# Optimization experiments

Hardware: AMD Instinct MI355X
Metric: run time of the kernel (lower is better)

The kernel has to match this reference:

```python
import jax, jax.numpy as jnp
import numpy as np

B, N, C, K = 2, 20000, 256, 16
H = C // 2  # gate hidden

def _ln(x, g, b, eps=1e-5):
    m = jnp.mean(x, axis=-1, keepdims=True)
    v = jnp.mean((x - m) ** 2, axis=-1, keepdims=True)
    return (x - m) * jax.lax.rsqrt(v + eps) * g + b

def setup_inputs() -> dict:
    key = jax.random.key(0)
    ks = jax.random.split(key, 16)
    s = 0.02
    return {
        'x_l0': jax.random.normal(ks[0], (B, N, C), jnp.float32),
        'x_l1': jax.random.normal(ks[1], (B, N, C), jnp.float32),
        'x_l2': jax.random.normal(ks[2], (B, N, C), jnp.float32),
        'x_l3': jax.random.normal(ks[3], (B, N, C), jnp.float32),
        'knn_idx': jax.random.randint(ks[4], (N, K), 0, N, jnp.int32),
        'Wq': jax.random.normal(ks[5], (3, C, C), jnp.float32) * s,
        'bq': jnp.zeros((3, C), jnp.float32),
        'Wk': jax.random.normal(ks[6], (3, C, C), jnp.float32) * s,
        'bk': jnp.zeros((3, C), jnp.float32),
        'Wv': jax.random.normal(ks[7], (3, C, C), jnp.float32) * s,
        'bv': jnp.zeros((3, C), jnp.float32),
        'ln_g': jnp.ones((3, C), jnp.float32),
        'ln_b': jnp.zeros((3, C), jnp.float32),
        'Wg1': jax.random.normal(ks[8], (H, C), jnp.float32) * s,
        'bg1': jnp.zeros((H,), jnp.float32),
        'Wg2': jax.random.normal(ks[9], (3, H), jnp.float32) * s,
        'bg2': jnp.zeros((3,), jnp.float32),
        'fn_g': jnp.ones((C,), jnp.float32),
        'fn_b': jnp.zeros((C,), jnp.float32),
    }

def reference(x_l0, x_l1, x_l2, x_l3, knn_idx, Wq, bq, Wk, bk, Wv, bv,
              ln_g, ln_b, Wg1, bg1, Wg2, bg2, fn_g, fn_b):
    c = x_l3.shape[-1]
    scale = 1.0 / jnp.sqrt(jnp.asarray(c, x_l3.dtype))

    def block(xq, i):
        Q = xq @ Wq[i].T + bq[i]            # (B,N,C)
        Kf = x_l3 @ Wk[i].T + bk[i]         # (B,N,C)
        Vf = x_l3 @ Wv[i].T + bv[i]
        Kk = Kf[:, knn_idx]                 # (B,N,K,C) gather along node dim
        Vk = Vf[:, knn_idx]
        s = jnp.einsum('bnc,bnkc->bnk', Q, Kk) * scale
        a = jax.nn.softmax(s, axis=-1)
        o = jnp.einsum('bnk,bnkc->bnc', a, Vk)
        return _ln(o + Q, ln_g[i], ln_b[i])

    Os = [block(x, i) for i, x in enumerate((x_l0, x_l1, x_l2))]
    h = jax.nn.relu(x_l3 @ Wg1.T + bg1)
    alpha = jax.nn.softmax(h @ Wg2.T + bg2, axis=-1)  # (B,N,3)
    out = sum(alpha[..., i:i + 1] * Os[i] for i in range(3))
    return _ln(out + x_l3, fn_g, fn_b)
```

## Files before the change

### kernel.cpp

```cpp
#include <hip/hip_runtime.h>

#define B_ 2
#define N_ 20000
#define C_ 256
#define K_ 16
#define H_ 128
#define ROWS (B_ * N_)
#define MT 313
#define MPAD (MT * 128)

typedef __attribute__((ext_vector_type(8))) short bf16x8;
typedef __attribute__((ext_vector_type(4))) float f32x4;

__device__ __forceinline__ float us2f(unsigned short u) {
    return __uint_as_float(((unsigned int)u) << 16);
}
__device__ __forceinline__ unsigned short f2us(float f) {
    unsigned int u = __float_as_uint(f);
    unsigned int r = (u + 0x7fffu + ((u >> 16) & 1u)) >> 16;
    return (unsigned short)r;
}
__device__ __forceinline__ float wred(float v) {
#pragma unroll
    for (int off = 32; off > 0; off >>= 1) v += __shfl_xor(v, off, 64);
    return v;
}
__device__ __forceinline__ void gld_lds16(const unsigned short* g, unsigned short* l) {
    __builtin_amdgcn_global_load_lds(
        (__attribute__((address_space(1))) void*)(g),
        (__attribute__((address_space(3))) void*)(l), 16, 0, 0);
}

extern "C" __global__ void __launch_bounds__(256)
cvt_kernel(const float* __restrict__ src, unsigned short* __restrict__ dst, int n4) {
    int t = blockIdx.x * 256 + threadIdx.x;
    if (t >= n4) return;
    float4 v = ((const float4*)src)[t];
    ushort4 o;
    o.x = f2us(v.x); o.y = f2us(v.y); o.z = f2us(v.z); o.w = f2us(v.w);
    ((ushort4*)dst)[t] = o;
}

extern "C" __global__ void __launch_bounds__(256)
cvtw_kernel(const float* __restrict__ s0, const float* __restrict__ s1,
            const float* __restrict__ s2, const float* __restrict__ s3,
            unsigned short* __restrict__ d0, unsigned short* __restrict__ d1,
            unsigned short* __restrict__ d2, unsigned short* __restrict__ d3) {
    const int y = blockIdx.y;
    const float* src = (y == 0) ? s0 : (y == 1 ? s1 : (y == 2 ? s2 : s3));
    unsigned short* dst = (y == 0) ? d0 : (y == 1 ? d1 : (y == 2 ? d2 : d3));
    const int n4 = (y < 3) ? (3 * C_ * C_ / 4) : (H_ * C_ / 4);
    int t = blockIdx.x * 256 + threadIdx.x;
    if (t >= n4) return;
    float4 v = ((const float4*)src)[t];
    ushort4 o;
    o.x = f2us(v.x); o.y = f2us(v.y); o.z = f2us(v.z); o.w = f2us(v.w);
    ((ushort4*)dst)[t] = o;
}

extern "C" __global__ void __launch_bounds__(256)
gemm_bf16(const unsigned short* __restrict__ A0, const unsigned short* __restrict__ A12,
          const unsigned short* __restrict__ W0, const unsigned short* __restrict__ W1,
          const unsigned short* __restrict__ W2, const float* __restrict__ b0,
          const float* __restrict__ b1, const float* __restrict__ b2,
          unsigned short* __restrict__ O0, unsigned short* __restrict__ O1,
          unsigned short* __restrict__ O2, const int Mvalid, const int ldo) {
    const int z = blockIdx.z;
    const unsigned short* A = (z == 0) ? A0 : A12;
    const unsigned short* W = (z == 0) ? W0 : (z == 1 ? W1 : W2);
    const float* bias = (z == 0) ? b0 : (z == 1 ? b1 : b2);
    unsigned short* O = (z == 0) ? O0 : (z == 1 ? O1 : O2);

    const int m0 = blockIdx.x * 128;
    const int n0 = blockIdx.y * 128;
    const int tid = threadIdx.x;
    const int w = tid >> 6, lane = tid & 63;
    const int l15 = lane & 15, l4 = lane >> 4;
    const int rowq = (w >> 1) * 64;
    const int colq = (w & 1) * 64;

    __shared__ unsigned short As[128 * 32];
    __shared__ unsigned short Bs[128 * 32];

    f32x4 acc[4][4] = {};

    const int srow = w * 16 + (lane >> 2);
    const int schunk = (lane & 3) * 8;

    for (int k0 = 0; k0 < 256; k0 += 32) {
        __syncthreads();
#pragma unroll
        for (int issue = 0; issue < 2; ++issue) {
            const int ra = m0 + issue * 64 + srow;
            const int rb = n0 + issue * 64 + srow;
            gld_lds16(A + (size_t)ra * 256 + k0 + schunk, As + issue * 2048 + w * 512);
            gld_lds16(W + (size_t)rb * 256 + k0 + schunk, Bs + issue * 2048 + w * 512);
        }
        __syncthreads();
        bf16x8 a[4], b[4];
#pragma unroll
        for (int i = 0; i < 4; ++i)
            a[i] = *(const bf16x8*)&As[(rowq + i * 16 + l15) * 32 + l4 * 8];
#pragma unroll
        for (int j = 0; j < 4; ++j)
            b[j] = *(const bf16x8*)&Bs[(colq + j * 16 + l15) * 32 + l4 * 8];
#pragma unroll
        for (int i = 0; i < 4; ++i)
#pragma unroll
            for (int j = 0; j < 4; ++j)
                acc[i][j] = __builtin_amdgcn_mfma_f32_16x16x32_bf16(a[i], b[j], acc[i][j], 0, 0, 0);
    }

#pragma unroll
    for (int j = 0; j < 4; ++j) {
        const int gcol = n0 + colq + j * 16 + l15;
        const float bj = bias[gcol];
#pragma unroll
        for (int i = 0; i < 4; ++i) {
#pragma unroll
            for (int r = 0; r < 4; ++r) {
                const int grow = m0 + rowq + i * 16 + l4 * 4 + r;
                if (grow < Mvalid) O[(size_t)grow * ldo + gcol] = f2us(acc[i][j][r] + bj);
            }
        }
    }
}

extern "C" __global__ void __launch_bounds__(256)
gate2_kernel(const unsigned short* __restrict__ Hbf, const float* __restrict__ Wg2,
             const float* __restrict__ bg2, float* __restrict__ alpha) {
    const int tid = threadIdx.x;
    const int w = tid >> 6, lane = tid & 63;
    const int row = blockIdx.x * 4 + w;
    const float h0 = fmaxf(us2f(Hbf[(size_t)row * H_ + lane]), 0.f);
    const float h1 = fmaxf(us2f(Hbf[(size_t)row * H_ + 64 + lane]), 0.f);
    float lg[3];
#pragma unroll
    for (int l = 0; l < 3; ++l) {
        const float* w2 = Wg2 + l * H_;
        lg[l] = wred(h0 * w2[lane] + h1 * w2[lane + 64]) + bg2[l];
    }
    float m = fmaxf(lg[0], fmaxf(lg[1], lg[2]));
    float e0 = expf(lg[0] - m), e1 = expf(lg[1] - m), e2 = expf(lg[2] - m);
    float inv = 1.f / (e0 + e1 + e2);
    if (lane == 0) {
        alpha[row * 3 + 0] = e0 * inv;
        alpha[row * 3 + 1] = e1 * inv;
        alpha[row * 3 + 2] = e2 * inv;
    }
}

extern "C" __global__ void __launch_bounds__(256)
attn_kernel(const unsigned short* __restrict__ q, const unsigned short* __restrict__ kf,
            const unsigned short* __restrict__ vf, const int* __restrict__ knn,
            const float* __restrict__ alpha, const float* __restrict__ lng,
            const float* __restrict__ lnb, float* __restrict__ accum, const int iblk) {
    const int tid = threadIdx.x;
    const int g = tid >> 4;
    const int t = tid & 15;
    const int row = blockIdx.x * 16 + g;
    const int b = row / N_;
    const int n = row - b * N_;

    float qv[16];
    const unsigned short* qp = q + (size_t)row * C_ + t * 4;
#pragma unroll
    for (int j = 0; j < 4; ++j) {
        ushort4 u = *(const ushort4*)(qp + j * 64);
        qv[j * 4 + 0] = us2f(u.x);
        qv[j * 4 + 1] = us2f(u.y);
        qv[j * 4 + 2] = us2f(u.z);
        qv[j * 4 + 3] = us2f(u.w);
    }

    int idxs[K_];
    float s[K_];
#pragma unroll
    for (int k = 0; k < K_; ++k) {
        idxs[k] = knn[n * K_ + k];
        const unsigned short* kp = kf + ((size_t)b * N_ + idxs[k]) * C_ + t * 4;
        float p = 0.f;
#pragma unroll
        for (int j = 0; j < 4; ++j) {
            ushort4 u = *(const ushort4*)(kp + j * 64);
            p += qv[j * 4 + 0] * us2f(u.x) + qv[j * 4 + 1] * us2f(u.y) +
                 qv[j * 4 + 2] * us2f(u.z) + qv[j * 4 + 3] * us2f(u.w);
        }
#pragma unroll
        for (int off = 1; off < 16; off <<= 1) p += __shfl_xor(p, off, 64);
        s[k] = p * 0.0625f;
    }

    float m = s[0];
#pragma unroll
    for (int k = 1; k < K_; ++k) m = fmaxf(m, s[k]);
    float sum = 0.f;
#pragma unroll
    for (int k = 0; k < K_; ++k) {
        s[k] = __expf(s[k] - m);
        sum += s[k];
    }
    const float inv = 1.f / sum;

    float o[16] = {};
#pragma unroll
    for (int k = 0; k < K_; ++k) {
        const float a = s[k] * inv;
        const unsigned short* vp = vf + ((size_t)b * N_ + idxs[k]) * C_ + t * 4;
#pragma unroll
        for (int j = 0; j < 4; ++j) {
            ushort4 u = *(const ushort4*)(vp + j * 64);
            o[j * 4 + 0] += a * us2f(u.x);
            o[j * 4 + 1] += a * us2f(u.y);
            o[j * 4 + 2] += a * us2f(u.z);
            o[j * 4 + 3] += a * us2f(u.w);
        }
    }

    float r[16];
    float s1 = 0.f, s2 = 0.f;
#pragma unroll
    for (int c = 0; c < 16; ++c) {
        r[c] = o[c] + qv[c];
        s1 += r[c];
        s2 += r[c] * r[c];
    }
#pragma unroll
    for (int off = 1; off < 16; off <<= 1) {
        s1 += __shfl_xor(s1, off, 64);
        s2 += __shfl_xor(s2, off, 64);
    }
    const float mean = s1 * (1.f / C_);
    const float var = s2 * (1.f / C_) - mean * mean;
    const float rstd = rsqrtf(var + 1e-5f);

    const float a = alpha[row * 3 + iblk];
    const float* gp = lng + iblk * C_ + t * 4;
    const float* bp = lnb + iblk * C_ + t * 4;
    float* ap = accum + (size_t)row * C_ + t * 4;
#pragma unroll
    for (int j = 0; j < 4; ++j) {
        float4 gg = *(const float4*)(gp + j * 64);
        float4 bb = *(const float4*)(bp + j * 64);
        float4 y;
        y.x = ((r[j * 4 + 0] - mean) * rstd * gg.x + bb.x) * a;
        y.y = ((r[j * 4 + 1] - mean) * rstd * gg.y + bb.y) * a;
        y.z = ((r[j * 4 + 2] - mean) * rstd * gg.z + bb.z) * a;
        y.w = ((r[j * 4 + 3] - mean) * rstd * gg.w + bb.w) * a;
        if (iblk == 0) {
            *(float4*)(ap + j * 64) = y;
        } else {
            float4 p = *(const float4*)(ap + j * 64);
            p.x += y.x; p.y += y.y; p.z += y.z; p.w += y.w;
            *(float4*)(ap + j * 64) = p;
        }
    }
}

extern "C" __global__ void __launch_bounds__(256)
final_kernel(float* __restrict__ accum, const float* __restrict__ x3,
             const float* __restrict__ fng, const float* __restrict__ fnb) {
    const int tid = threadIdx.x;
    const int w = tid >> 6, lane = tid & 63;
    const int row = blockIdx.x * 4 + w;
    const int c0 = lane * 4;
    float4 a = *(const float4*)(accum + (size_t)row * C_ + c0);
    float4 xv = *(const float4*)(x3 + (size_t)row * C_ + c0);
    float4 r = make_float4(a.x + xv.x, a.y + xv.y, a.z + xv.z, a.w + xv.w);
    float s1 = wred(r.x + r.y + r.z + r.w);
    float s2 = wred(r.x * r.x + r.y * r.y + r.z * r.z + r.w * r.w);
    const float mean = s1 * (1.f / C_);
    const float var = s2 * (1.f / C_) - mean * mean;
    const float rstd = rsqrtf(var + 1e-5f);
    const float* g = fng + c0;
    const float* bb = fnb + c0;
    float4 y;
    y.x = (r.x - mean) * rstd * g[0] + bb[0];
    y.y = (r.y - mean) * rstd * g[1] + bb[1];
    y.z = (r.z - mean) * rstd * g[2] + bb[2];
    y.w = (r.w - mean) * rstd * g[3] + bb[3];
    *(float4*)(accum + (size_t)row * C_ + c0) = y;
}

extern "C" void kernel_launch(void* const* d_in, const int* in_sizes, int n_in,
                              void* d_out, int out_size, void* d_ws, size_t ws_size,
                              hipStream_t stream) {
    const float* x0 = (const float*)d_in[0];
    const float* x1 = (const float*)d_in[1];
    const float* x2 = (const float*)d_in[2];
    const float* x3 = (const float*)d_in[3];
    const int* knn = (const int*)d_in[4];
    const float* Wq = (const float*)d_in[5];
    const float* bq = (const float*)d_in[6];
    const float* Wk = (const float*)d_in[7];
    const float* bk = (const float*)d_in[8];
    const float* Wv = (const float*)d_in[9];
    const float* bv = (const float*)d_in[10];
    const float* ln_g = (const float*)d_in[11];
    const float* ln_b = (const float*)d_in[12];
    const float* Wg1 = (const float*)d_in[13];
    const float* bg1 = (const float*)d_in[14];
    const float* Wg2 = (const float*)d_in[15];
    const float* bg2 = (const float*)d_in[16];
    const float* fn_g = (const float*)d_in[17];
    const float* fn_b = (const float*)d_in[18];
    float* out = (float*)d_out;

    unsigned char* w8 = (unsigned char*)d_ws;
    const size_t XBF = (size_t)MPAD * C_ * 2;
    const size_t HBF = (size_t)MPAD * H_ * 2;
    const size_t WBLOB = (size_t)3 * C_ * C_ * 2;
    unsigned short* x3bf = (unsigned short*)(w8);
    unsigned short* xqbf = (unsigned short*)(w8 + XBF);
    unsigned short* qbf  = (unsigned short*)(w8 + 2 * XBF);
    unsigned short* kbf  = (unsigned short*)(w8 + 3 * XBF);
    unsigned short* vbf  = (unsigned short*)(w8 + 4 * XBF);
    unsigned short* Hbf  = (unsigned short*)(w8 + 5 * XBF);
    unsigned short* wqbf = (unsigned short*)(w8 + 5 * XBF + HBF);
    unsigned short* wkbf = (unsigned short*)(w8 + 5 * XBF + HBF + WBLOB);
    unsigned short* wvbf = (unsigned short*)(w8 + 5 * XBF + HBF + 2 * WBLOB);
    unsigned short* wg1bf = (unsigned short*)(w8 + 5 * XBF + HBF + 3 * WBLOB);
    float* alpha = (float*)(w8 + 5 * XBF + HBF + 3 * WBLOB + (size_t)H_ * C_ * 2);

    const int xn4 = ROWS * C_ / 4;
    const int wn4 = 3 * C_ * C_ / 4;

    cvt_kernel<<<(xn4 + 255) / 256, 256, 0, stream>>>(x3, x3bf, xn4);
    cvtw_kernel<<<dim3((wn4 + 255) / 256, 4), 256, 0, stream>>>(
        Wq, Wk, Wv, Wg1, wqbf, wkbf, wvbf, wg1bf);

    gemm_bf16<<<dim3(MT, 1, 1), 256, 0, stream>>>(
        x3bf, x3bf, wg1bf, wg1bf, wg1bf, bg1, bg1, bg1, Hbf, Hbf, Hbf, ROWS, H_);
    gate2_kernel<<<ROWS / 4, 256, 0, stream>>>(Hbf, Wg2, bg2, alpha);

    const float* xq[3] = {x0, x1, x2};
    for (int i = 0; i < 3; ++i) {
        cvt_kernel<<<(xn4 + 255) / 256, 256, 0, stream>>>(xq[i], xqbf, xn4);
        gemm_bf16<<<dim3(MT, 2, 3), 256, 0, stream>>>(
            xqbf, x3bf, wqbf + (size_t)i * C_ * C_, wkbf + (size_t)i * C_ * C_,
            wvbf + (size_t)i * C_ * C_, bq + i * C_, bk + i * C_, bv + i * C_,
            qbf, kbf, vbf, ROWS, C_);
        attn_kernel<<<ROWS / 16, 256, 0, stream>>>(qbf, kbf, vbf, knn, alpha,
                                                   ln_g, ln_b, out, i);
    }
    final_kernel<<<ROWS / 4, 256, 0, stream>>>(out, x3, fn_g, fn_b);
}
```

Measured before the change: 672.8 us.

## Fuse three attention blocks and final layernorm into one gather kernel

Stores Q/K/V for all three blocks in separate workspace slices so a single attn3 kernel can process all three blocks per row. The kernel accumulates the alpha-weighted layernormed outputs in registers and applies the final residual layernorm directly. This removes the fp32 read-modify-write of the output accumulator across three passes and the separate final kernel launch. It also reuses the loaded neighbour indices and uses 8-wide bf16 loads. The cost is roughly twice the workspace, and the old path is kept as a fallback when the workspace is too small.

```diff
diff --git a/kernel.cpp b/kernel.cpp
--- a/kernel.cpp
+++ b/kernel.cpp
@@ -10,6 +10,7 @@
 #define MPAD (MT * 128)
 
 typedef __attribute__((ext_vector_type(8))) short bf16x8;
+typedef __attribute__((ext_vector_type(8))) unsigned short us8;
 typedef __attribute__((ext_vector_type(4))) float f32x4;
 
 __device__ __forceinline__ float us2f(unsigned short u) {
@@ -147,6 +148,174 @@
         alpha[row * 3 + 0] = e0 * inv;
         alpha[row * 3 + 1] = e1 * inv;
         alpha[row * 3 + 2] = e2 * inv;
+    }
+}
+
+extern "C" __global__ void __launch_bounds__(256)
+attn3_kernel(const unsigned short* __restrict__ qb, const unsigned short* __restrict__ kb,
+             const unsigned short* __restrict__ vb, const int* __restrict__ knn,
+             const float* __restrict__ alpha, const float* __restrict__ lng,
+             const float* __restrict__ lnb, const float* __restrict__ x3,
+             const float* __restrict__ fng, const float* __restrict__ fnb,
+             float* __restrict__ out) {
+    const int tid = threadIdx.x;
+    const int t = tid & 15;
+    const int row = blockIdx.x * 16 + (tid >> 4);
+    const int b = row / N_;
+    const int n = row - b * N_;
+    const int XE = MPAD * C_;
+
+    int goff[K_];
+    {
+        const int4* kn = (const int4*)(knn + n * K_);
+#pragma unroll
+        for (int k4 = 0; k4 < 4; ++k4) {
+            int4 v = kn[k4];
+            const int base = b * N_;
+            goff[k4 * 4 + 0] = (base + v.x) * C_ + t * 8;
+            goff[k4 * 4 + 1] = (base + v.y) * C_ + t * 8;
+            goff[k4 * 4 + 2] = (base + v.z) * C_ + t * 8;
+            goff[k4 * 4 + 3] = (base + v.w) * C_ + t * 8;
+        }
+    }
+
+    float acc[16] = {};
+
+#pragma unroll 1
+    for (int i = 0; i < 3; ++i) {
+        const unsigned short* q  = qb + (size_t)i * XE;
+        const unsigned short* kf = kb + (size_t)i * XE;
+        const unsigned short* vf = vb + (size_t)i * XE;
+
+        float qv[16];
+        const unsigned short* qp = q + (size_t)row * C_ + t * 8;
+#pragma unroll
+        for (int j = 0; j < 2; ++j) {
+            us8 u = *(const us8*)(qp + j * 128);
+#pragma unroll
+            for (int e = 0; e < 8; ++e) qv[j * 8 + e] = us2f(u[e]);
+        }
+
+        float s[K_];
+#pragma unroll
+        for (int k = 0; k < K_; ++k) {
+            const unsigned short* kp = kf + goff[k];
+            float p = 0.f;
+#pragma unroll
+            for (int j = 0; j < 2; ++j) {
+                us8 u = *(const us8*)(kp + j * 128);
+#pragma unroll
+                for (int e = 0; e < 8; ++e) p += qv[j * 8 + e] * us2f(u[e]);
+            }
+#pragma unroll
+            for (int off = 1; off < 16; off <<= 1) p += __shfl_xor(p, off, 64);
+            s[k] = p * 0.0625f;
+        }
+
+        float m = s[0];
+#pragma unroll
+        for (int k = 1; k < K_; ++k) m = fmaxf(m, s[k]);
+        float sum = 0.f;
+#pragma unroll
+        for (int k = 0; k < K_; ++k) {
+            s[k] = __expf(s[k] - m);
+            sum += s[k];
+        }
+        const float inv = 1.f / sum;
+
+        float o[16] = {};
+#pragma unroll
+        for (int k = 0; k < K_; ++k) {
+            const float a = s[k] * inv;
+            const unsigned short* vp = vf + goff[k];
+#pragma unroll
+            for (int j = 0; j < 2; ++j) {
+                us8 u = *(const us8*)(vp + j * 128);
+#pragma unroll
+                for (int e = 0; e < 8; ++e) o[j * 8 + e] += a * us2f(u[e]);
+            }
+        }
+
+        float s1 = 0.f, s2 = 0.f;
+#pragma unroll
+        for (int c = 0; c < 16; ++c) {
+            o[c] += qv[c];
+            s1 += o[c];
+            s2 += o[c] * o[c];
+        }
+#pragma unroll
+        for (int off = 1; off < 16; off <<= 1) {
+            s1 += __shfl_xor(s1, off, 64);
+            s2 += __shfl_xor(s2, off, 64);
+        }
+        const float mean = s1 * (1.f / C_);
+        const float var = s2 * (1.f / C_) - mean * mean;
+        const float rstd = rsqrtf(var + 1e-5f);
+
+        const float a = alpha[row * 3 + i];
+        const float* gp = lng + i * C_ + t * 8;
+        const float* bp = lnb + i * C_ + t * 8;
+#pragma unroll
+        for (int j = 0; j < 2; ++j) {
+#pragma unroll
+            for (int h = 0; h < 2; ++h) {
+                float4 gg = *(const float4*)(gp + j * 128 + h * 4);
+                float4 bb = *(const float4*)(bp + j * 128 + h * 4);
+                const int ci = j * 8 + h * 4;
+                acc[ci + 0] += ((o[ci + 0] - mean) * rstd * gg.x + bb.x) * a;
+                acc[ci + 1] += ((o[ci + 1] - mean) * rstd * gg.y + bb.y) * a;
+                acc[ci + 2] += ((o[ci + 2] - mean) * rstd * gg.z + bb.z) * a;
+                acc[ci + 3] += ((o[ci + 3] - mean) * rstd * gg.w + bb.w) * a;
+            }
+        }
+    }
+
+    const float* xp = x3 + (size_t)row * C_ + t * 8;
+    float r[16];
+    float s1 = 0.f, s2 = 0.f;
+#pragma unroll
+    for (int j = 0; j < 2; ++j) {
+#pragma unroll
+        for (int h = 0; h < 2; ++h) {
+            float4 xv = *(const float4*)(xp + j * 128 + h * 4);
+            const int ci = j * 8 + h * 4;
+            r[ci + 0] = acc[ci + 0] + xv.x;
+            r[ci + 1] = acc[ci + 1] + xv.y;
+            r[ci + 2] = acc[ci + 2] + xv.z;
+            r[ci + 3] = acc[ci + 3] + xv.w;
+        }
+    }
+#pragma unroll
+    for (int c = 0; c < 16; ++c) {
+        s1 += r[c];
+        s2 += r[c] * r[c];
+    }
+#pragma unroll
+    for (int off = 1; off < 16; off <<= 1) {
+        s1 += __shfl_xor(s1, off, 64);
+        s2 += __shfl_xor(s2, off, 64);
+    }
+    const float mean = s1 * (1.f / C_);
+    const float var = s2 * (1.f / C_) - mean * mean;
+    const float rstd = rsqrtf(var + 1e-5f);
+
+    const float* gp = fng + t * 8;
+    const float* bp = fnb + t * 8;
+    float* op = out + (size_t)row * C_ + t * 8;
+#pragma unroll
+    for (int j = 0; j < 2; ++j) {
+#pragma unroll
+        for (int h = 0; h < 2; ++h) {
+            float4 gg = *(const float4*)(gp + j * 128 + h * 4);
+            float4 bb = *(const float4*)(bp + j * 128 + h * 4);
+            const int ci = j * 8 + h * 4;
+            float4 y;
+            y.x = (r[ci + 0] - mean) * rstd * gg.x + bb.x;
+            y.y = (r[ci + 1] - mean) * rstd * gg.y + bb.y;
+            y.z = (r[ci + 2] - mean) * rstd * gg.z + bb.z;
+            y.w = (r[ci + 3] - mean) * rstd * gg.w + bb.w;
+            *(float4*)(op + j * 128 + h * 4) = y;
+        }
     }
 }
 
@@ -310,38 +479,76 @@
     const size_t XBF = (size_t)MPAD * C_ * 2;
     const size_t HBF = (size_t)MPAD * H_ * 2;
     const size_t WBLOB = (size_t)3 * C_ * C_ * 2;
-    unsigned short* x3bf = (unsigned short*)(w8);
-    unsigned short* xqbf = (unsigned short*)(w8 + XBF);
-    unsigned short* qbf  = (unsigned short*)(w8 + 2 * XBF);
-    unsigned short* kbf  = (unsigned short*)(w8 + 3 * XBF);
-    unsigned short* vbf  = (unsigned short*)(w8 + 4 * XBF);
-    unsigned short* Hbf  = (unsigned short*)(w8 + 5 * XBF);
-    unsigned short* wqbf = (unsigned short*)(w8 + 5 * XBF + HBF);
-    unsigned short* wkbf = (unsigned short*)(w8 + 5 * XBF + HBF + WBLOB);
-    unsigned short* wvbf = (unsigned short*)(w8 + 5 * XBF + HBF + 2 * WBLOB);
-    unsigned short* wg1bf = (unsigned short*)(w8 + 5 * XBF + HBF + 3 * WBLOB);
-    float* alpha = (float*)(w8 + 5 * XBF + HBF + 3 * WBLOB + (size_t)H_ * C_ * 2);
+    const size_t WG1B = (size_t)H_ * C_ * 2;
+    const size_t ALPHAB = (size_t)ROWS * 3 * 4;
 
     const int xn4 = ROWS * C_ / 4;
     const int wn4 = 3 * C_ * C_ / 4;
-
-    cvt_kernel<<<(xn4 + 255) / 256, 256, 0, stream>>>(x3, x3bf, xn4);
-    cvtw_kernel<<<dim3((wn4 + 255) / 256, 4), 256, 0, stream>>>(
-        Wq, Wk, Wv, Wg1, wqbf, wkbf, wvbf, wg1bf);
-
-    gemm_bf16<<<dim3(MT, 1, 1), 256, 0, stream>>>(
-        x3bf, x3bf, wg1bf, wg1bf, wg1bf, bg1, bg1, bg1, Hbf, Hbf, Hbf, ROWS, H_);
-    gate2_kernel<<<ROWS / 4, 256, 0, stream>>>(Hbf, Wg2, bg2, alpha);
-
     const float* xq[3] = {x0, x1, x2};
-    for (int i = 0; i < 3; ++i) {
-        cvt_kernel<<<(xn4 + 255) / 256, 256, 0, stream>>>(xq[i], xqbf, xn4);
-        gemm_bf16<<<dim3(MT, 2, 3), 256, 0, stream>>>(
-            xqbf, x3bf, wqbf + (size_t)i * C_ * C_, wkbf + (size_t)i * C_ * C_,
-            wvbf + (size_t)i * C_ * C_, bq + i * C_, bk + i * C_, bv + i * C_,
-            qbf, kbf, vbf, ROWS, C_);
-        attn_kernel<<<ROWS / 16, 256, 0, stream>>>(qbf, kbf, vbf, knn, alpha,
-                                                   ln_g, ln_b, out, i);
-    }
-    final_kernel<<<ROWS / 4, 256, 0, stream>>>(out, x3, fn_g, fn_b);
-}
+
+    const size_t NEED_FUSED = 11 * XBF + HBF + 3 * WBLOB + WG1B + ALPHAB;
+
+    if (ws_size >= NEED_FUSED) {
+        unsigned short* x3bf = (unsigned short*)(w8);
+        unsigned short* xqbf = (unsigned short*)(w8 + XBF);
+        unsigned short* qbf  = (unsigned short*)(w8 + 2 * XBF);
+        unsigned short* kbf  = (unsigned short*)(w8 + 5 * XBF);
+        unsigned short* vbf  = (unsigned short*)(w8 + 8 * XBF);
+        unsigned short* Hbf  = (unsigned short*)(w8 + 11 * XBF);
+        unsigned short* wqbf = (unsigned short*)(w8 + 11 * XBF + HBF);
+        unsigned short* wkbf = (unsigned short*)(w8 + 11 * XBF + HBF + WBLOB);
+        unsigned short* wvbf = (unsigned short*)(w8 + 11 * XBF + HBF + 2 * WBLOB);
+        unsigned short* wg1bf = (unsigned short*)(w8 + 11 * XBF + HBF + 3 * WBLOB);
+        float* alpha = (float*)(w8 + 11 * XBF + HBF + 3 * WBLOB + WG1B);
+        const size_t XE = (size_t)MPAD * C_;
+
+        cvt_kernel<<<(xn4 + 255) / 256, 256, 0, stream>>>(x3, x3bf, xn4);
+        cvtw_kernel<<<dim3((wn4 + 255) / 256, 4), 256, 0, stream>>>(
+            Wq, Wk, Wv, Wg1, wqbf, wkbf, wvbf, wg1bf);
+
+        gemm_bf16<<<dim3(MT, 1, 1), 256, 0, stream>>>(
+            x3bf, x3bf, wg1bf, wg1bf, wg1bf, bg1, bg1, bg1, Hbf, Hbf, Hbf, ROWS, H_);
+        gate2_kernel<<<ROWS / 4, 256, 0, stream>>>(Hbf, Wg2, bg2, alpha);
+
+        for (int i = 0; i < 3; ++i) {
+            cvt_kernel<<<(xn4 + 255) / 256, 256, 0, stream>>>(xq[i], xqbf, xn4);
+            gemm_bf16<<<dim3(MT, 2, 3), 256, 0, stream>>>(
+                xqbf, x3bf, wqbf + (size_t)i * C_ * C_, wkbf + (size_t)i * C_ * C_,
+                wvbf + (size_t)i * C_ * C_, bq + i * C_, bk + i * C_, bv + i * C_,
+                qbf + i * XE, kbf + i * XE, vbf + i * XE, ROWS, C_);
+        }
+        attn3_kernel<<<ROWS / 16, 256, 0, stream>>>(qbf, kbf, vbf, knn, alpha,
+                                                    ln_g, ln_b, x3, fn_g, fn_b, out);
+    } else {
+        unsigned short* x3bf = (unsigned short*)(w8);
+        unsigned short* xqbf = (unsigned short*)(w8 + XBF);
+        unsigned short* qbf  = (unsigned short*)(w8 + 2 * XBF);
+        unsigned short* kbf  = (unsigned short*)(w8 + 3 * XBF);
+        unsigned short* vbf  = (unsigned short*)(w8 + 4 * XBF);
+        unsigned short* Hbf  = (unsigned short*)(w8 + 5 * XBF);
+        unsigned short* wqbf = (unsigned short*)(w8 + 5 * XBF + HBF);
+        unsigned short* wkbf = (unsigned short*)(w8 + 5 * XBF + HBF + WBLOB);
+        unsigned short* wvbf = (unsigned short*)(w8 + 5 * XBF + HBF + 2 * WBLOB);
+        unsigned short* wg1bf = (unsigned short*)(w8 + 5 * XBF + HBF + 3 * WBLOB);
+        float* alpha = (float*)(w8 + 5 * XBF + HBF + 3 * WBLOB + WG1B);
+
+        cvt_kernel<<<(xn4 + 255) / 256, 256, 0, stream>>>(x3, x3bf, xn4);
+        cvtw_kernel<<<dim3((wn4 + 255) / 256, 4), 256, 0, stream>>>(
+            Wq, Wk, Wv, Wg1, wqbf, wkbf, wvbf, wg1bf);
+
+        gemm_bf16<<<dim3(MT, 1, 1), 256, 0, stream>>>(
+            x3bf, x3bf, wg1bf, wg1bf, wg1bf, bg1, bg1, bg1, Hbf, Hbf, Hbf, ROWS, H_);
+        gate2_kernel<<<ROWS / 4, 256, 0, stream>>>(Hbf, Wg2, bg2, alpha);
+
+        for (int i = 0; i < 3; ++i) {
+            cvt_kernel<<<(xn4 + 255) / 256, 256, 0, stream>>>(xq[i], xqbf, xn4);
+            gemm_bf16<<<dim3(MT, 2, 3), 256, 0, stream>>>(
+                xqbf, x3bf, wqbf + (size_t)i * C_ * C_, wkbf + (size_t)i * C_ * C_,
+                wvbf + (size_t)i * C_ * C_, bq + i * C_, bk + i * C_, bv + i * C_,
+                qbf, kbf, vbf, ROWS, C_);
+            attn_kernel<<<ROWS / 16, 256, 0, stream>>>(qbf, kbf, vbf, knn, alpha,
+                                                       ln_g, ln_b, out, i);
+        }
+        final_kernel<<<ROWS / 4, 256, 0, stream>>>(out, x3, fn_g, fn_b);
+    }
+}
```

Measured after the change: 910.5 us. 35.3% more time.

## Batch input conversions, fuse final layernorm into last attention pass

Applied to the files above, without the earlier changes.

Converts x3 and all three query inputs to bf16 in one 2D-grid launch instead of four separate launches, using extra workspace for the three query buffers. The final layernorm (residual add with x3 and the fn_g/fn_b normalisation) moves into the third attention kernel, which removes a separate read-modify-write pass over the output. Two attention variants get different minimum-occupancy launch bounds (6 and 5 waves), which may cap registers and cause spills. The workspace footprint grows by two activation-sized buffers.

```diff
diff --git a/kernel.cpp b/kernel.cpp
--- a/kernel.cpp
+++ b/kernel.cpp
@@ -32,7 +32,12 @@
 }
 
 extern "C" __global__ void __launch_bounds__(256)
-cvt_kernel(const float* __restrict__ src, unsigned short* __restrict__ dst, int n4) {
+cvtx_kernel(const float* __restrict__ x3, const float* __restrict__ x0,
+            const float* __restrict__ x1, const float* __restrict__ x2,
+            unsigned short* __restrict__ d3, unsigned short* __restrict__ dq, int n4) {
+    const int y = blockIdx.y;
+    const float* src = (y == 0) ? x3 : (y == 1 ? x0 : (y == 2 ? x1 : x2));
+    unsigned short* dst = (y == 0) ? d3 : (dq + (size_t)(y - 1) * MPAD * C_);
     int t = blockIdx.x * 256 + threadIdx.x;
     if (t >= n4) return;
     float4 v = ((const float4*)src)[t];
@@ -150,19 +155,11 @@
     }
 }
 
-extern "C" __global__ void __launch_bounds__(256)
-attn_kernel(const unsigned short* __restrict__ q, const unsigned short* __restrict__ kf,
-            const unsigned short* __restrict__ vf, const int* __restrict__ knn,
-            const float* __restrict__ alpha, const float* __restrict__ lng,
-            const float* __restrict__ lnb, float* __restrict__ accum, const int iblk) {
-    const int tid = threadIdx.x;
-    const int g = tid >> 4;
-    const int t = tid & 15;
-    const int row = blockIdx.x * 16 + g;
-    const int b = row / N_;
-    const int n = row - b * N_;
-
-    float qv[16];
+__device__ __forceinline__ void attn_core(
+    const unsigned short* __restrict__ q, const unsigned short* __restrict__ kf,
+    const unsigned short* __restrict__ vf, const int* __restrict__ knn,
+    const int row, const int b, const int n, const int t,
+    float* __restrict__ qv, float* __restrict__ o) {
     const unsigned short* qp = q + (size_t)row * C_ + t * 4;
 #pragma unroll
     for (int j = 0; j < 4; ++j) {
@@ -202,7 +199,8 @@
     }
     const float inv = 1.f / sum;
 
-    float o[16] = {};
+#pragma unroll
+    for (int c = 0; c < 16; ++c) o[c] = 0.f;
 #pragma unroll
     for (int k = 0; k < K_; ++k) {
         const float a = s[k] * inv;
@@ -216,14 +214,19 @@
             o[j * 4 + 3] += a * us2f(u.w);
         }
     }
-
-    float r[16];
+}
+
+__device__ __forceinline__ void attn_epilogue(
+    const float* __restrict__ alpha, const float* __restrict__ lng,
+    const float* __restrict__ lnb, float* __restrict__ accum,
+    const int iblk, const int row, const int t,
+    float* __restrict__ qv, float* __restrict__ o) {
     float s1 = 0.f, s2 = 0.f;
 #pragma unroll
     for (int c = 0; c < 16; ++c) {
-        r[c] = o[c] + qv[c];
-        s1 += r[c];
-        s2 += r[c] * r[c];
+        o[c] += qv[c];
+        s1 += o[c];
+        s2 += o[c] * o[c];
     }
 #pragma unroll
     for (int off = 1; off < 16; off <<= 1) {
@@ -243,10 +246,10 @@
         float4 gg = *(const float4*)(gp + j * 64);
         float4 bb = *(const float4*)(bp + j * 64);
         float4 y;
-        y.x = ((r[j * 4 + 0] - mean) * rstd * gg.x + bb.x) * a;
-        y.y = ((r[j * 4 + 1] - mean) * rstd * gg.y + bb.y) * a;
-        y.z = ((r[j * 4 + 2] - mean) * rstd * gg.z + bb.z) * a;
-        y.w = ((r[j * 4 + 3] - mean) * rstd * gg.w + bb.w) * a;
+        y.x = ((o[j * 4 + 0] - mean) * rstd * gg.x + bb.x) * a;
+        y.y = ((o[j * 4 + 1] - mean) * rstd * gg.y + bb.y) * a;
+        y.z = ((o[j * 4 + 2] - mean) * rstd * gg.z + bb.z) * a;
+        y.w = ((o[j * 4 + 3] - mean) * rstd * gg.w + bb.w) * a;
         if (iblk == 0) {
             *(float4*)(ap + j * 64) = y;
         } else {
@@ -257,29 +260,112 @@
     }
 }
 
+extern "C" __global__ void __launch_bounds__(256, 6)
+attn_w6(const unsigned short* __restrict__ q, const unsigned short* __restrict__ kf,
+        const unsigned short* __restrict__ vf, const int* __restrict__ knn,
+        const float* __restrict__ alpha, const float* __restrict__ lng,
+        const float* __restrict__ lnb, float* __restrict__ accum, const int iblk) {
+    const int tid = threadIdx.x;
+    const int t = tid & 15;
+    const int row = blockIdx.x * 16 + (tid >> 4);
+    const int b = row / N_;
+    const int n = row - b * N_;
+    float qv[16], o[16];
+    attn_core(q, kf, vf, knn, row, b, n, t, qv, o);
+    attn_epilogue(alpha, lng, lnb, accum, iblk, row, t, qv, o);
+}
+
 extern "C" __global__ void __launch_bounds__(256)
-final_kernel(float* __restrict__ accum, const float* __restrict__ x3,
-             const float* __restrict__ fng, const float* __restrict__ fnb) {
+attn_base(const unsigned short* __restrict__ q, const unsigned short* __restrict__ kf,
+          const unsigned short* __restrict__ vf, const int* __restrict__ knn,
+          const float* __restrict__ alpha, const float* __restrict__ lng,
+          const float* __restrict__ lnb, float* __restrict__ accum, const int iblk) {
     const int tid = threadIdx.x;
-    const int w = tid >> 6, lane = tid & 63;
-    const int row = blockIdx.x * 4 + w;
-    const int c0 = lane * 4;
-    float4 a = *(const float4*)(accum + (size_t)row * C_ + c0);
-    float4 xv = *(const float4*)(x3 + (size_t)row * C_ + c0);
-    float4 r = make_float4(a.x + xv.x, a.y + xv.y, a.z + xv.z, a.w + xv.w);
-    float s1 = wred(r.x + r.y + r.z + r.w);
-    float s2 = wred(r.x * r.x + r.y * r.y + r.z * r.z + r.w * r.w);
+    const int t = tid & 15;
+    const int row = blockIdx.x * 16 + (tid >> 4);
+    const int b = row / N_;
+    const int n = row - b * N_;
+    float qv[16], o[16];
+    attn_core(q, kf, vf, knn, row, b, n, t, qv, o);
+    attn_epilogue(alpha, lng, lnb, accum, iblk, row, t, qv, o);
+}
+
+extern "C" __global__ void __launch_bounds__(256, 5)
+attn_last(const unsigned short* __restrict__ q, const unsigned short* __restrict__ kf,
+          const unsigned short* __restrict__ vf, const int* __restrict__ knn,
+          const float* __restrict__ alpha, const float* __restrict__ lng,
+          const float* __restrict__ lnb, const float* __restrict__ accum,
+          const float* __restrict__ x3, const float* __restrict__ fng,
+          const float* __restrict__ fnb, float* __restrict__ out) {
+    const int tid = threadIdx.x;
+    const int t = tid & 15;
+    const int row = blockIdx.x * 16 + (tid >> 4);
+    const int b = row / N_;
+    const int n = row - b * N_;
+    float qv[16], o[16];
+    attn_core(q, kf, vf, knn, row, b, n, t, qv, o);
+
+    float s1 = 0.f, s2 = 0.f;
+#pragma unroll
+    for (int c = 0; c < 16; ++c) {
+        o[c] += qv[c];
+        s1 += o[c];
+        s2 += o[c] * o[c];
+    }
+#pragma unroll
+    for (int off = 1; off < 16; off <<= 1) {
+        s1 += __shfl_xor(s1, off, 64);
+        s2 += __shfl_xor(s2, off, 64);
+    }
     const float mean = s1 * (1.f / C_);
     const float var = s2 * (1.f / C_) - mean * mean;
     const float rstd = rsqrtf(var + 1e-5f);
-    const float* g = fng + c0;
-    const float* bb = fnb + c0;
-    float4 y;
-    y.x = (r.x - mean) * rstd * g[0] + bb[0];
-    y.y = (r.y - mean) * rstd * g[1] + bb[1];
-    y.z = (r.z - mean) * rstd * g[2] + bb[2];
-    y.w = (r.w - mean) * rstd * g[3] + bb[3];
-    *(float4*)(accum + (size_t)row * C_ + c0) = y;
+
+    const float a = alpha[row * 3 + 2];
+    const float* gp = lng + 2 * C_ + t * 4;
+    const float* bp = lnb + 2 * C_ + t * 4;
+    const float* ap = accum + (size_t)row * C_ + t * 4;
+    const float* xp = x3 + (size_t)row * C_ + t * 4;
+    float u1 = 0.f, u2 = 0.f;
+#pragma unroll
+    for (int j = 0; j < 4; ++j) {
+        float4 gg = *(const float4*)(gp + j * 64);
+        float4 bb = *(const float4*)(bp + j * 64);
+        float4 pa = *(const float4*)(ap + j * 64);
+        float4 xv = *(const float4*)(xp + j * 64);
+        o[j * 4 + 0] = pa.x + xv.x + ((o[j * 4 + 0] - mean) * rstd * gg.x + bb.x) * a;
+        o[j * 4 + 1] = pa.y + xv.y + ((o[j * 4 + 1] - mean) * rstd * gg.y + bb.y) * a;
+        o[j * 4 + 2] = pa.z + xv.z + ((o[j * 4 + 2] - mean) * rstd * gg.z + bb.z) * a;
+        o[j * 4 + 3] = pa.w + xv.w + ((o[j * 4 + 3] - mean) * rstd * gg.w + bb.w) * a;
+    }
+#pragma unroll
+    for (int c = 0; c < 16; ++c) {
+        u1 += o[c];
+        u2 += o[c] * o[c];
+    }
+#pragma unroll
+    for (int off = 1; off < 16; off <<= 1) {
+        u1 += __shfl_xor(u1, off, 64);
+        u2 += __shfl_xor(u2, off, 64);
+    }
+    const float fmean = u1 * (1.f / C_);
+    const float fvar = u2 * (1.f / C_) - fmean * fmean;
+    const float frstd = rsqrtf(fvar + 1e-5f);
+
+    const float* fgp = fng + t * 4;
+    const float* fbp = fnb + t * 4;
+    float* op = out + (size_t)row * C_ + t * 4;
+#pragma unroll
+    for (int j = 0; j < 4; ++j) {
+        float4 gg = *(const float4*)(fgp + j * 64);
+        float4 bb = *(const float4*)(fbp + j * 64);
+        float4 y;
+        y.x = (o[j * 4 + 0] - fmean) * frstd * gg.x + bb.x;
+        y.y = (o[j * 4 + 1] - fmean) * frstd * gg.y + bb.y;
+        y.z = (o[j * 4 + 2] - fmean) * frstd * gg.z + bb.z;
+        y.w = (o[j * 4 + 3] - fmean) * frstd * gg.w + bb.w;
+        *(float4*)(op + j * 64) = y;
+    }
 }
 
 extern "C" void kernel_launch(void* const* d_in, const int* in_sizes, int n_in,
@@ -310,22 +396,26 @@
     const size_t XBF = (size_t)MPAD * C_ * 2;
     const size_t HBF = (size_t)MPAD * H_ * 2;
     const size_t WBLOB = (size_t)3 * C_ * C_ * 2;
-    unsigned short* x3bf = (unsigned short*)(w8);
-    unsigned short* xqbf = (unsigned short*)(w8 + XBF);
-    unsigned short* qbf  = (unsigned short*)(w8 + 2 * XBF);
-    unsigned short* kbf  = (unsigned short*)(w8 + 3 * XBF);
-    unsigned short* vbf  = (unsigned short*)(w8 + 4 * XBF);
-    unsigned short* Hbf  = (unsigned short*)(w8 + 5 * XBF);
-    unsigned short* wqbf = (unsigned short*)(w8 + 5 * XBF + HBF);
-    unsigned short* wkbf = (unsigned short*)(w8 + 5 * XBF + HBF + WBLOB);
-    unsigned short* wvbf = (unsigned short*)(w8 + 5 * XBF + HBF + 2 * WBLOB);
-    unsigned short* wg1bf = (unsigned short*)(w8 + 5 * XBF + HBF + 3 * WBLOB);
-    float* alpha = (float*)(w8 + 5 * XBF + HBF + 3 * WBLOB + (size_t)H_ * C_ * 2);
+    const size_t WG1B = (size_t)H_ * C_ * 2;
+    const size_t XE = (size_t)MPAD * C_;
+
+    unsigned short* x3bf  = (unsigned short*)(w8);
+    unsigned short* xqall = (unsigned short*)(w8 + XBF);
+    unsigned short* qbf   = (unsigned short*)(w8 + 4 * XBF);
+    unsigned short* kbf   = (unsigned short*)(w8 + 5 * XBF);
+    unsigned short* vbf   = (unsigned short*)(w8 + 6 * XBF);
+    unsigned short* Hbf   = (unsigned short*)(w8 + 7 * XBF);
+    unsigned short* wqbf  = (unsigned short*)(w8 + 7 * XBF + HBF);
+    unsigned short* wkbf  = (unsigned short*)(w8 + 7 * XBF + HBF + WBLOB);
+    unsigned short* wvbf  = (unsigned short*)(w8 + 7 * XBF + HBF + 2 * WBLOB);
+    unsigned short* wg1bf = (unsigned short*)(w8 + 7 * XBF + HBF + 3 * WBLOB);
+    float* alpha = (float*)(w8 + 7 * XBF + HBF + 3 * WBLOB + WG1B);
 
     const int xn4 = ROWS * C_ / 4;
     const int wn4 = 3 * C_ * C_ / 4;
 
-    cvt_kernel<<<(xn4 + 255) / 256, 256, 0, stream>>>(x3, x3bf, xn4);
+    cvtx_kernel<<<dim3((xn4 + 255) / 256, 4), 256, 0, stream>>>(
+        x3, x0, x1, x2, x3bf, xqall, xn4);
     cvtw_kernel<<<dim3((wn4 + 255) / 256, 4), 256, 0, stream>>>(
         Wq, Wk, Wv, Wg1, wqbf, wkbf, wvbf, wg1bf);
 
@@ -333,15 +423,22 @@
         x3bf, x3bf, wg1bf, wg1bf, wg1bf, bg1, bg1, bg1, Hbf, Hbf, Hbf, ROWS, H_);
     gate2_kernel<<<ROWS / 4, 256, 0, stream>>>(Hbf, Wg2, bg2, alpha);
 
-    const float* xq[3] = {x0, x1, x2};
     for (int i = 0; i < 3; ++i) {
-        cvt_kernel<<<(xn4 + 255) / 256, 256, 0, stream>>>(xq[i], xqbf, xn4);
         gemm_bf16<<<dim3(MT, 2, 3), 256, 0, stream>>>(
-            xqbf, x3bf, wqbf + (size_t)i * C_ * C_, wkbf + (size_t)i * C_ * C_,
+            xqall + (size_t)i * XE, x3bf,
+            wqbf + (size_t)i * C_ * C_, wkbf + (size_t)i * C_ * C_,
             wvbf + (size_t)i * C_ * C_, bq + i * C_, bk + i * C_, bv + i * C_,
             qbf, kbf, vbf, ROWS, C_);
-        attn_kernel<<<ROWS / 16, 256, 0, stream>>>(qbf, kbf, vbf, knn, alpha,
-                                                   ln_g, ln_b, out, i);
-    }
-    final_kernel<<<ROWS / 4, 256, 0, stream>>>(out, x3, fn_g, fn_b);
-}
+        if (i == 0) {
+            attn_w6<<<ROWS / 16, 256, 0, stream>>>(qbf, kbf, vbf, knn, alpha,
+                                                   ln_g, ln_b, out, 0);
+        } else if (i == 1) {
+            attn_base<<<ROWS / 16, 256, 0, stream>>>(qbf, kbf, vbf, knn, alpha,
+                                                     ln_g, ln_b, out, 1);
+        } else {
+            attn_last<<<ROWS / 16, 256, 0, stream>>>(qbf, kbf, vbf, knn, alpha,
+                                                     ln_g, ln_b, out, x3,
+                                                     fn_g, fn_b, out);
+        }
+    }
+}
```

Result: slower. 886.4 us (+31.7%).
